# Optimization experiments

Hardware: AMD Instinct MI355X
Metric: run time of the kernel (lower is better)

Reference implementation:

```python
import jax, jax.numpy as jnp
import numpy as np

B, S, D, H = 64, 197, 1024, 4096

# I-BERT IntGELU constants: erf(x) ~ a*(x+b)^2 + c on [0,-b], integer-only form
K_SQRT2 = 1.4142          # sqrt(2)
GELU_SHIFT = 14           # 2**14 right-shift to avoid accumulator overflow
COEF_A = -0.2888
COEF_B = -1.769
COEF_C = 1.0 / COEF_A     # c folded by a, as in I-BERT (coeff[2] /= coeff[0])


def setup_inputs() -> dict:
    key = jax.random.key(0)
    k1, k2, k3, k4, k5, k6 = jax.random.split(key, 6)
    x_int = jax.random.randint(k1, (B, S, D), 0, 127).astype(jnp.int32)  # int8-range activations
    s_x = jax.random.uniform(k2, (1,), jnp.float32, 0.01, 0.03)          # per-tensor act scale
    w1 = jax.random.normal(k3, (H, D), jnp.float32) * 0.02
    b1 = jax.random.normal(k4, (H,), jnp.float32) * 0.02
    w2 = jax.random.normal(k5, (D, H), jnp.float32) * 0.02
    b2 = jax.random.normal(k6, (D,), jnp.float32) * 0.02
    return {"x_int": x_int, "s_x": s_x, "w1": w1, "b1": b1, "w2": w2, "b2": b2}


def _quant_weight(w):
    # per-tensor symmetric int8 weight quantization (QuantLinearWithWeight)
    s_w = jnp.max(jnp.abs(w)) / 127.0
    w_int = jnp.clip(jnp.round(w / s_w), -127.0, 127.0)
    return w_int, s_w


def _quant_linear(x_int, s_x, w, b):
    # integer GEMM: int8 acts x int8 weights -> int32 accumulator, scale s_x*s_w
    w_int, s_w = _quant_weight(w)
    s_out = s_x * s_w
    b_int = jnp.round(b / s_out)  # bias quantized into the accumulator scale
    acc = jnp.einsum('bsd,hd->bsh', x_int, w_int) + b_int
    return acc, s_out


def _int_erf(x_int, sf):
    # integer polynomial approx of erf (I-BERT)
    b_int = jnp.floor(COEF_B / sf)
    c_int = jnp.floor(COEF_C / sf ** 2)
    sign = jnp.sign(x_int)
    abs_int = jnp.minimum(jnp.abs(x_int), -b_int)
    y_int = sign * ((abs_int + b_int) ** 2 + c_int)
    sf_out = sf ** 2 * COEF_A
    y_int = jnp.floor(y_int / 2.0 ** GELU_SHIFT)  # shift to keep accumulator in range
    return y_int, sf_out * 2.0 ** GELU_SHIFT


def _int_gelu(x_int, sf):
    # GELU(x) = x * 0.5 * (1 + erf(x/sqrt(2))), integer-only
    sig_int, sig_sf = _int_erf(x_int, sf / K_SQRT2)
    shift_int = jnp.floor(1.0 / sig_sf)  # torch: 1.0 // sigmoid_scaling_factor
    y_int = x_int * (sig_int + shift_int)
    return y_int, sf * sig_sf / 2.0


def _quant_act(x_int, sf):
    # QuantAct: requantize int32-scale activations back to int8 (dynamic per-tensor scale)
    x_hat = x_int * sf
    s_a = jnp.max(jnp.abs(x_hat)) / 127.0
    q = jnp.clip(jnp.round(x_hat / s_a), -128.0, 127.0)
    return q, s_a


def reference(x_int, s_x, w1, b1, w2, b2):
    x = x_int.astype(jnp.float32)
    s = s_x[0]
    x, s = _quant_linear(x, s, w1, b1)   # [B,S,H] int32 accumulator
    x, s = _int_gelu(x, s)               # integer-only GELU
    x, s = _quant_act(x, s)              # requant -> int8 range
    # dropout_1 is identity in eval mode
    x, s = _quant_linear(x, s, w2, b2)   # [B,S,D] int32 accumulator
    # dropout_2 is identity in eval mode
    return x, s
```

## Files before the change

### kernel.cpp

```cpp
#include <hip/hip_runtime.h>
#include <cstdint>
#include <cstddef>

constexpr int Bb = 64, Ss = 197, Dd = 1024, Hh = 4096;
constexpr int M  = Bb * Ss;
constexpr int MT = (M + 255) / 256;
constexpr int Mpad = MT * 256;
constexpr int NBLK1 = (Hh / 256) * MT;

#define SL_S1    4
#define SL_BERF  5
#define SL_CERF  6
#define SL_SHIFT 7
#define SL_S2    8
#define SL_SA    9
#define SL_SOUT2 10
#define SL_SW1   11
#define SL_SW2   12

typedef int v4i __attribute__((ext_vector_type(4)));

#define GLD_LDS(g, l) \
  __builtin_amdgcn_global_load_lds((const __attribute__((address_space(1))) void*)(g), \
                                   (__attribute__((address_space(3))) void*)(l), 16, 0, 0)

#define PBAR() asm volatile("s_barrier" ::: "memory")
#define SCHED_FENCE() __builtin_amdgcn_sched_barrier(0)

__device__ __forceinline__ float blockmax256(float m) {
  #pragma unroll
  for (int off = 32; off; off >>= 1) m = fmaxf(m, __shfl_down(m, off, 64));
  __shared__ float wm[4];
  int lane = threadIdx.x & 63, wid = threadIdx.x >> 6;
  if (lane == 0) wm[wid] = m;
  __syncthreads();
  return fmaxf(fmaxf(wm[0], wm[1]), fmaxf(wm[2], wm[3]));
}

__global__ void k_wmax(const float* __restrict__ w1, const float* __restrict__ w2,
                       int n4, float* __restrict__ pmax) {
  int b = blockIdx.x;
  const float4* s4 = (const float4*)(b < 512 ? w1 : w2);
  float m = 0.f;
  for (int i = (b & 511) * 256 + threadIdx.x; i < n4; i += 512 * 256) {
    float4 v = s4[i];
    m = fmaxf(m, fmaxf(fmaxf(fabsf(v.x), fabsf(v.y)), fmaxf(fabsf(v.z), fabsf(v.w))));
  }
  m = blockmax256(m);
  if (threadIdx.x == 0) pmax[b] = m;
}

__global__ void k_scalars1(unsigned* slu, const float* __restrict__ pmax,
                           const float* __restrict__ s_x_ptr) {
  int t = threadIdx.x;
  float m1 = fmaxf(pmax[t], pmax[t + 256]);
  float m2 = fmaxf(pmax[512 + t], pmax[768 + t]);
  __shared__ float r1[256], r2[256];
  r1[t] = m1; r2[t] = m2;
  __syncthreads();
  for (int s = 128; s; s >>= 1) {
    if (t < s) { r1[t] = fmaxf(r1[t], r1[t + s]); r2[t] = fmaxf(r2[t], r2[t + s]); }
    __syncthreads();
  }
  if (t == 0) {
    float* slf = (float*)slu;
    float s_w1 = r1[0] / 127.0f;
    float s_w2 = r2[0] / 127.0f;
    float s1  = s_x_ptr[0] * s_w1;
    float sfe = s1 / 1.4142f;
    float berf = floorf(-1.769f / sfe);
    float cerf = floorf(((float)(1.0 / -0.2888)) / (sfe * sfe));
    float sig  = ((sfe * sfe) * -0.2888f) * 16384.0f;
    float shiftv = floorf(1.0f / sig);
    float s2 = (s1 * sig) / 2.0f;
    slf[SL_S1] = s1; slf[SL_BERF] = berf; slf[SL_CERF] = cerf;
    slf[SL_SHIFT] = shiftv; slf[SL_S2] = s2; slf[SL_SW1] = s_w1; slf[SL_SW2] = s_w2;
  }
}

__global__ void k_scalars2(unsigned* slu, const float* __restrict__ pmax,
                           float* dout_scalar) {
  int t = threadIdx.x;
  float m = 0.f;
  for (int i = t; i < NBLK1; i += 256) m = fmaxf(m, pmax[i]);
  __shared__ float r1[256];
  r1[t] = m;
  __syncthreads();
  for (int s = 128; s; s >>= 1) {
    if (t < s) r1[t] = fmaxf(r1[t], r1[t + s]);
    __syncthreads();
  }
  if (t == 0) {
    float* slf = (float*)slu;
    float xm = fabsf(r1[0] * slf[SL_S2]);
    float sa = xm / 127.0f;
    float sout2 = sa * slf[SL_SW2];
    slf[SL_SA] = sa; slf[SL_SOUT2] = sout2;
    *dout_scalar = sout2;
  }
}

__global__ void k_quantcvt(const float* __restrict__ w1, const float* __restrict__ w2,
                           const int* __restrict__ x, const unsigned* __restrict__ slu,
                           int8_t* __restrict__ w1q, int8_t* __restrict__ w2q,
                           int8_t* __restrict__ xq) {
  const float* slf = (const float*)slu;
  float sw1 = slf[SL_SW1], sw2 = slf[SL_SW2];
  const int n1 = Hh * Dd / 4, n2 = Dd * Hh / 4;
  const int nx = M * Dd / 4, n3 = Mpad * Dd / 4;
  const int total = n1 + n2 + n3;
  for (int i = blockIdx.x * blockDim.x + threadIdx.x; i < total; i += gridDim.x * blockDim.x) {
    if (i < n1 + n2) {
      bool first = i < n1;
      int idx = first ? i : i - n1;
      float sw = first ? sw1 : sw2;
      float4 v = ((const float4*)(first ? w1 : w2))[idx];
      int qa = (int)fminf(fmaxf(rintf(v.x / sw), -127.f), 127.f);
      int qb = (int)fminf(fmaxf(rintf(v.y / sw), -127.f), 127.f);
      int qc = (int)fminf(fmaxf(rintf(v.z / sw), -127.f), 127.f);
      int qd = (int)fminf(fmaxf(rintf(v.w / sw), -127.f), 127.f);
      unsigned p = (unsigned)(qa & 0xff) | ((unsigned)(qb & 0xff) << 8) |
                   ((unsigned)(qc & 0xff) << 16) | ((unsigned)(qd & 0xff) << 24);
      ((unsigned*)(first ? w1q : w2q))[idx] = p;
    } else {
      int idx = i - n1 - n2;
      unsigned p = 0u;
      if (idx < nx) {
        int4 v = ((const int4*)x)[idx];
        p = (unsigned)(v.x & 0xff) | ((unsigned)(v.y & 0xff) << 8) |
            ((unsigned)(v.z & 0xff) << 16) | ((unsigned)(v.w & 0xff) << 24);
      }
      ((unsigned*)xq)[idx] = p;
    }
  }
}

template <int K, int MODE>
__global__ __launch_bounds__(512, 2) void k_gemm(
    const int8_t* __restrict__ A, const int8_t* __restrict__ Bm,
    const float* __restrict__ bias, const unsigned* __restrict__ slu,
    int8_t* __restrict__ qout, float* __restrict__ fout, float* __restrict__ pmax_y,
    int Mreal, int Ncols) {
  constexpr int NK = K / 128;
  __shared__ alignas(64) int8_t smem[131072];
  const int t = threadIdx.x;
  const int bm = blockIdx.y, bn = blockIdx.x;
  const int lane = t & 63, wid = t >> 6;
  const int wr = wid >> 2, wc = wid & 3;
  const int lm = lane & 15, quad = lane >> 4;

  const int srow = t >> 2;
  const int scc  = (t & 3) ^ ((srow >> 1) & 3);
  const int8_t* aSrc = A  + (size_t)(bm * 256 + srow) * K + scc * 16;
  const int8_t* bSrc = Bm + (size_t)(bn * 256 + srow) * K + scc * 16;

  int aoff[8], boff[4];
  #pragma unroll
  for (int i = 0; i < 8; i++) {
    int r = wr * 128 + i * 16 + lm;
    aoff[i] = r * 64 + ((quad ^ ((r >> 1) & 3)) << 4);
  }
  #pragma unroll
  for (int j = 0; j < 4; j++) {
    int r = wc * 64 + j * 16 + lm;
    boff[j] = r * 64 + ((quad ^ ((r >> 1) & 3)) << 4);
  }

  v4i acc[8][4] = {};

  auto stA = [&](int buf, int kt, int ks) {
    int8_t* d = smem + buf * 65536 + ks * 16384 + t * 16;
    const int8_t* s = aSrc + kt * 128 + ks * 64;
    GLD_LDS(s, d);
    GLD_LDS(s + (size_t)128 * K, d + 8192);
  };
  auto stB = [&](int buf, int kt, int ks) {
    int8_t* d = smem + buf * 65536 + 32768 + ks * 16384 + t * 16;
    const int8_t* s = bSrc + kt * 128 + ks * 64;
    GLD_LDS(s, d);
    GLD_LDS(s + (size_t)128 * K, d + 8192);
  };

  stB(0, 0, 0); stA(0, 0, 0); stB(0, 0, 1); stA(0, 0, 1);
  asm volatile("s_waitcnt vmcnt(4)" ::: "memory");
  SCHED_FENCE();
  PBAR();

  #pragma unroll 1
  for (int kt = 0; kt < NK; ++kt) {
    const int cb = kt & 1, nb = cb ^ 1;
    const int8_t* Ac = smem + cb * 65536;
    const int8_t* Bc = Ac + 32768;
    const bool pf = (kt + 1 < NK);
    v4i bf[4], af[4];

    #pragma unroll
    for (int j = 0; j < 4; j++) bf[j] = *(const v4i*)(Bc + boff[j]);
    #pragma unroll
    for (int i = 0; i < 4; i++) af[i] = *(const v4i*)(Ac + aoff[i]);
    if (pf) stB(nb, kt + 1, 0);
    PBAR();
    __builtin_amdgcn_s_setprio(1);
    #pragma unroll
    for (int i = 0; i < 4; i++)
      #pragma unroll
      for (int j = 0; j < 4; j++)
        acc[i][j] = __builtin_amdgcn_mfma_i32_16x16x64_i8(bf[j], af[i], acc[i][j], 0, 0, 0);
    __builtin_amdgcn_s_setprio(0);
    SCHED_FENCE();
    PBAR();

    #pragma unroll
    for (int i = 0; i < 4; i++) af[i] = *(const v4i*)(Ac + aoff[4 + i]);
    if (pf) stA(nb, kt + 1, 0);
    PBAR();
    __builtin_amdgcn_s_setprio(1);
    #pragma unroll
    for (int i = 0; i < 4; i++)
      #pragma unroll
      for (int j = 0; j < 4; j++)
        acc[4 + i][j] = __builtin_amdgcn_mfma_i32_16x16x64_i8(bf[j], af[i], acc[4 + i][j], 0, 0, 0);
    __builtin_amdgcn_s_setprio(0);
    if (pf) asm volatile("s_waitcnt vmcnt(4)" ::: "memory");
    else    asm volatile("s_waitcnt vmcnt(0)" ::: "memory");
    SCHED_FENCE();
    PBAR();

    #pragma unroll
    for (int j = 0; j < 4; j++) bf[j] = *(const v4i*)(Bc + 16384 + boff[j]);
    #pragma unroll
    for (int i = 0; i < 4; i++) af[i] = *(const v4i*)(Ac + 16384 + aoff[i]);
    if (pf) stB(nb, kt + 1, 1);
    PBAR();
    __builtin_amdgcn_s_setprio(1);
    #pragma unroll
    for (int i = 0; i < 4; i++)
      #pragma unroll
      for (int j = 0; j < 4; j++)
        acc[i][j] = __builtin_amdgcn_mfma_i32_16x16x64_i8(bf[j], af[i], acc[i][j], 0, 0, 0);
    __builtin_amdgcn_s_setprio(0);
    SCHED_FENCE();
    PBAR();

    #pragma unroll
    for (int i = 0; i < 4; i++) af[i] = *(const v4i*)(Ac + 16384 + aoff[4 + i]);
    if (pf) stA(nb, kt + 1, 1);
    PBAR();
    __builtin_amdgcn_s_setprio(1);
    #pragma unroll
    for (int i = 0; i < 4; i++)
      #pragma unroll
      for (int j = 0; j < 4; j++)
        acc[4 + i][j] = __builtin_amdgcn_mfma_i32_16x16x64_i8(bf[j], af[i], acc[4 + i][j], 0, 0, 0);
    __builtin_amdgcn_s_setprio(0);
    if (pf) asm volatile("s_waitcnt vmcnt(4)" ::: "memory");
    else    asm volatile("s_waitcnt vmcnt(0)" ::: "memory");
    SCHED_FENCE();
    PBAR();
  }

  const float* slf = (const float*)slu;
  if constexpr (MODE == 2) {
    float sout2 = slf[SL_SOUT2];
    float4 bq[4];
    #pragma unroll
    for (int j = 0; j < 4; j++) {
      float4 bv = *(const float4*)(bias + bn * 256 + wc * 64 + j * 16 + quad * 4);
      bq[j].x = rintf(bv.x / sout2); bq[j].y = rintf(bv.y / sout2);
      bq[j].z = rintf(bv.z / sout2); bq[j].w = rintf(bv.w / sout2);
    }
    #pragma unroll
    for (int i = 0; i < 8; i++) {
      int gr = bm * 256 + wr * 128 + i * 16 + lm;
      if (gr < Mreal) {
        #pragma unroll
        for (int j = 0; j < 4; j++) {
          int gc0 = bn * 256 + wc * 64 + j * 16 + quad * 4;
          float4 o;
          o.x = (float)acc[i][j][0] + bq[j].x;
          o.y = (float)acc[i][j][1] + bq[j].y;
          o.z = (float)acc[i][j][2] + bq[j].z;
          o.w = (float)acc[i][j][3] + bq[j].w;
          *(float4*)(fout + (size_t)gr * Ncols + gc0) = o;
        }
      }
    }
  } else {
    float s1 = slf[SL_S1], berf = slf[SL_BERF], cerf = slf[SL_CERF], shiftv = slf[SL_SHIFT];
    float s2 = slf[SL_S2];
    float sa = (MODE == 1) ? slf[SL_SA] : 1.0f;
    float r_req = (MODE == 1) ? (s2 / sa) : 1.0f;
    float lmax = 0.f;
    float4 bq[4];
    #pragma unroll
    for (int j = 0; j < 4; j++) {
      float4 bv = *(const float4*)(bias + bn * 256 + wc * 64 + j * 16 + quad * 4);
      bq[j].x = rintf(bv.x / s1); bq[j].y = rintf(bv.y / s1);
      bq[j].z = rintf(bv.z / s1); bq[j].w = rintf(bv.w / s1);
    }
    #pragma unroll
    for (int i = 0; i < 8; i++) {
      int mrow = wr * 128 + i * 16 + lm;
      int gr = bm * 256 + mrow;
      bool rowok = gr < Mreal;
      #pragma unroll
      for (int j = 0; j < 4; j++) {
        int n0 = wc * 64 + j * 16 + quad * 4;
        unsigned packed = 0u;
        #pragma unroll
        for (int r = 0; r < 4; r++) {
          float a = (float)acc[i][j][r] + ((const float*)&bq[j])[r];
          float ax = fminf(fabsf(a), -berf);
          float tt = ax + berf;
          float u = tt * tt + cerf;
          float ye = (a < 0.f) ? -u : u;
          float yv = floorf(ye * (1.0f / 16384.0f));
          float y = a * (yv + shiftv);
          if constexpr (MODE == 0) {
            if (rowok) lmax = fmaxf(lmax, fabsf(y));
          } else {
            float qf = rintf(y * r_req);
            qf = fminf(fmaxf(qf, -128.f), 127.f);
            packed |= ((unsigned)((int)qf & 0xff)) << (8 * r);
          }
        }
        if constexpr (MODE == 1) {
          *(unsigned*)(smem + mrow * 272 + n0) = packed;
        }
      }
    }
    if constexpr (MODE == 0) {
      #pragma unroll
      for (int off = 32; off; off >>= 1) lmax = fmaxf(lmax, __shfl_down(lmax, off, 64));
      float* red = (float*)smem;
      if (lane == 0) red[wid] = lmax;
      __syncthreads();
      if (t == 0) {
        float b = fmaxf(fmaxf(fmaxf(red[0], red[1]), fmaxf(red[2], red[3])),
                        fmaxf(fmaxf(red[4], red[5]), fmaxf(red[6], red[7])));
        pmax_y[bm * gridDim.x + bn] = b;
      }
    } else {
      __syncthreads();
      #pragma unroll
      for (int c2 = 0; c2 < 8; c2++) {
        int idx = c2 * 512 + t;
        int row = idx >> 4, c16 = (idx & 15) << 4;
        v4i v = *(const v4i*)(smem + row * 272 + c16);
        *(v4i*)(qout + (size_t)(bm * 256 + row) * Ncols + bn * 256 + c16) = v;
      }
    }
  }
}

extern "C" void kernel_launch(void* const* d_in, const int* in_sizes, int n_in,
                              void* d_out, int out_size, void* d_ws, size_t ws_size,
                              hipStream_t stream) {
  const int*   x   = (const int*)d_in[0];
  const float* s_x = (const float*)d_in[1];
  const float* w1  = (const float*)d_in[2];
  const float* b1  = (const float*)d_in[3];
  const float* w2  = (const float*)d_in[4];
  const float* b2  = (const float*)d_in[5];
  float* out = (float*)d_out;

  char* ws = (char*)d_ws;
  unsigned* slots = (unsigned*)ws;
  float* pmax_w = (float*)(ws + 1024);
  float* pmax_y = (float*)(ws + 8192);
  int8_t* w1q = (int8_t*)(ws + 32768);
  int8_t* w2q = w1q + (size_t)Hh * Dd;
  int8_t* xq  = w2q + (size_t)Dd * Hh;
  int8_t* qbuf = xq + (size_t)Mpad * Dd;

  k_wmax<<<1024, 256, 0, stream>>>(w1, w2, Hh * Dd / 4, pmax_w);
  k_scalars1<<<1, 256, 0, stream>>>(slots, pmax_w, s_x);
  k_quantcvt<<<1024, 256, 0, stream>>>(w1, w2, x, slots, w1q, w2q, xq);

  dim3 g1(Hh / 256, MT);
  k_gemm<Dd, 0><<<g1, 512, 0, stream>>>(xq, w1q, b1, slots, nullptr, nullptr,
                                        pmax_y, M, Hh);
  k_scalars2<<<1, 256, 0, stream>>>(slots, pmax_y, out + (size_t)M * Dd);
  k_gemm<Dd, 1><<<g1, 512, 0, stream>>>(xq, w1q, b1, slots, qbuf, nullptr,
                                        nullptr, M, Hh);
  dim3 g2(Dd / 256, MT);
  k_gemm<Hh, 2><<<g2, 512, 0, stream>>>(qbuf, w2q, b2, slots, nullptr, out,
                                        nullptr, M, Dd);
}
```

Baseline: 383.9 us.

## Replace double-buffered interleaved GEMM pipeline with single-buffer 256-wide K tiles

Replaces the fine-grained double-buffered K loop (128-wide K tiles in two 64-wide halves, each load interleaved with MFMA work under raw barriers) with a single buffer holding 256-wide K tiles. The whole tile is loaded with 16-byte swizzled async copies, the kernel waits and syncs, runs all MFMAs, syncs again, and only then issues the next load. This makes the loop simpler and halves the number of iterations, but global loads no longer overlap with compute, so memory latency is exposed on every tile.

```diff
diff --git a/kernel.cpp b/kernel.cpp
--- a/kernel.cpp
+++ b/kernel.cpp
@@ -23,9 +23,6 @@
 #define GLD_LDS(g, l) \
   __builtin_amdgcn_global_load_lds((const __attribute__((address_space(1))) void*)(g), \
                                    (__attribute__((address_space(3))) void*)(l), 16, 0, 0)
-
-#define PBAR() asm volatile("s_barrier" ::: "memory")
-#define SCHED_FENCE() __builtin_amdgcn_sched_barrier(0)
 
 __device__ __forceinline__ float blockmax256(float m) {
   #pragma unroll
@@ -141,7 +138,7 @@
     const float* __restrict__ bias, const unsigned* __restrict__ slu,
     int8_t* __restrict__ qout, float* __restrict__ fout, float* __restrict__ pmax_y,
     int Mreal, int Ncols) {
-  constexpr int NK = K / 128;
+  constexpr int NK = K / 256;
   __shared__ alignas(64) int8_t smem[131072];
   const int t = threadIdx.x;
   const int bm = blockIdx.y, bn = blockIdx.x;
@@ -149,114 +146,65 @@
   const int wr = wid >> 2, wc = wid & 3;
   const int lm = lane & 15, quad = lane >> 4;
 
-  const int srow = t >> 2;
-  const int scc  = (t & 3) ^ ((srow >> 1) & 3);
-  const int8_t* aSrc = A  + (size_t)(bm * 256 + srow) * K + scc * 16;
-  const int8_t* bSrc = Bm + (size_t)(bn * 256 + srow) * K + scc * 16;
-
-  int aoff[8], boff[4];
+  const int srow0 = t >> 4;
+  const int gcol  = (t & 15) ^ (srow0 & 7);
+  const int8_t* aSrc = A  + (size_t)(bm * 256 + srow0) * K + gcol * 16;
+  const int8_t* bSrc = Bm + (size_t)(bn * 256 + srow0) * K + gcol * 16;
+
+  v4i acc[8][4] = {};
+
+  auto stage = [&](int kt) {
+    const size_t ko = (size_t)kt * 256;
+    #pragma unroll
+    for (int j = 0; j < 8; j++) {
+      GLD_LDS(aSrc + (size_t)(32 * j) * K + ko, smem + (j * 512 + t) * 16);
+      GLD_LDS(bSrc + (size_t)(32 * j) * K + ko, smem + 65536 + (j * 512 + t) * 16);
+    }
+  };
+
+  int arow[8], ar7[8], brow[4], br7[4];
   #pragma unroll
   for (int i = 0; i < 8; i++) {
     int r = wr * 128 + i * 16 + lm;
-    aoff[i] = r * 64 + ((quad ^ ((r >> 1) & 3)) << 4);
+    arow[i] = r * 256; ar7[i] = r & 7;
   }
   #pragma unroll
   for (int j = 0; j < 4; j++) {
     int r = wc * 64 + j * 16 + lm;
-    boff[j] = r * 64 + ((quad ^ ((r >> 1) & 3)) << 4);
-  }
-
-  v4i acc[8][4] = {};
-
-  auto stA = [&](int buf, int kt, int ks) {
-    int8_t* d = smem + buf * 65536 + ks * 16384 + t * 16;
-    const int8_t* s = aSrc + kt * 128 + ks * 64;
-    GLD_LDS(s, d);
-    GLD_LDS(s + (size_t)128 * K, d + 8192);
-  };
-  auto stB = [&](int buf, int kt, int ks) {
-    int8_t* d = smem + buf * 65536 + 32768 + ks * 16384 + t * 16;
-    const int8_t* s = bSrc + kt * 128 + ks * 64;
-    GLD_LDS(s, d);
-    GLD_LDS(s + (size_t)128 * K, d + 8192);
-  };
-
-  stB(0, 0, 0); stA(0, 0, 0); stB(0, 0, 1); stA(0, 0, 1);
-  asm volatile("s_waitcnt vmcnt(4)" ::: "memory");
-  SCHED_FENCE();
-  PBAR();
+    brow[j] = r * 256; br7[j] = r & 7;
+  }
+
+  stage(0);
 
   #pragma unroll 1
   for (int kt = 0; kt < NK; ++kt) {
-    const int cb = kt & 1, nb = cb ^ 1;
-    const int8_t* Ac = smem + cb * 65536;
-    const int8_t* Bc = Ac + 32768;
-    const bool pf = (kt + 1 < NK);
-    v4i bf[4], af[4];
-
-    #pragma unroll
-    for (int j = 0; j < 4; j++) bf[j] = *(const v4i*)(Bc + boff[j]);
-    #pragma unroll
-    for (int i = 0; i < 4; i++) af[i] = *(const v4i*)(Ac + aoff[i]);
-    if (pf) stB(nb, kt + 1, 0);
-    PBAR();
+    asm volatile("s_waitcnt vmcnt(0)");
+    __syncthreads();
+    const int8_t* As = smem;
+    const int8_t* Bs = smem + 65536;
     __builtin_amdgcn_s_setprio(1);
     #pragma unroll
-    for (int i = 0; i < 4; i++)
-      #pragma unroll
-      for (int j = 0; j < 4; j++)
-        acc[i][j] = __builtin_amdgcn_mfma_i32_16x16x64_i8(bf[j], af[i], acc[i][j], 0, 0, 0);
+    for (int ksub = 0; ksub < 4; ksub++) {
+      v4i af[8], bf[4];
+      #pragma unroll
+      for (int j = 0; j < 4; j++) {
+        int pc = ((ksub << 2) | quad) ^ br7[j];
+        bf[j] = *(const v4i*)(Bs + brow[j] + (pc << 4));
+      }
+      #pragma unroll
+      for (int i = 0; i < 8; i++) {
+        int pc = ((ksub << 2) | quad) ^ ar7[i];
+        af[i] = *(const v4i*)(As + arow[i] + (pc << 4));
+      }
+      #pragma unroll
+      for (int i = 0; i < 8; i++)
+        #pragma unroll
+        for (int j = 0; j < 4; j++)
+          acc[i][j] = __builtin_amdgcn_mfma_i32_16x16x64_i8(bf[j], af[i], acc[i][j], 0, 0, 0);
+    }
     __builtin_amdgcn_s_setprio(0);
-    SCHED_FENCE();
-    PBAR();
-
-    #pragma unroll
-    for (int i = 0; i < 4; i++) af[i] = *(const v4i*)(Ac + aoff[4 + i]);
-    if (pf) stA(nb, kt + 1, 0);
-    PBAR();
-    __builtin_amdgcn_s_setprio(1);
-    #pragma unroll
-    for (int i = 0; i < 4; i++)
-      #pragma unroll
-      for (int j = 0; j < 4; j++)
-        acc[4 + i][j] = __builtin_amdgcn_mfma_i32_16x16x64_i8(bf[j], af[i], acc[4 + i][j], 0, 0, 0);
-    __builtin_amdgcn_s_setprio(0);
-    if (pf) asm volatile("s_waitcnt vmcnt(4)" ::: "memory");
-    else    asm volatile("s_waitcnt vmcnt(0)" ::: "memory");
-    SCHED_FENCE();
-    PBAR();
-
-    #pragma unroll
-    for (int j = 0; j < 4; j++) bf[j] = *(const v4i*)(Bc + 16384 + boff[j]);
-    #pragma unroll
-    for (int i = 0; i < 4; i++) af[i] = *(const v4i*)(Ac + 16384 + aoff[i]);
-    if (pf) stB(nb, kt + 1, 1);
-    PBAR();
-    __builtin_amdgcn_s_setprio(1);
-    #pragma unroll
-    for (int i = 0; i < 4; i++)
-      #pragma unroll
-      for (int j = 0; j < 4; j++)
-        acc[i][j] = __builtin_amdgcn_mfma_i32_16x16x64_i8(bf[j], af[i], acc[i][j], 0, 0, 0);
-    __builtin_amdgcn_s_setprio(0);
-    SCHED_FENCE();
-    PBAR();
-
-    #pragma unroll
-    for (int i = 0; i < 4; i++) af[i] = *(const v4i*)(Ac + 16384 + aoff[4 + i]);
-    if (pf) stA(nb, kt + 1, 1);
-    PBAR();
-    __builtin_amdgcn_s_setprio(1);
-    #pragma unroll
-    for (int i = 0; i < 4; i++)
-      #pragma unroll
-      for (int j = 0; j < 4; j++)
-        acc[4 + i][j] = __builtin_amdgcn_mfma_i32_16x16x64_i8(bf[j], af[i], acc[4 + i][j], 0, 0, 0);
-    __builtin_amdgcn_s_setprio(0);
-    if (pf) asm volatile("s_waitcnt vmcnt(4)" ::: "memory");
-    else    asm volatile("s_waitcnt vmcnt(0)" ::: "memory");
-    SCHED_FENCE();
-    PBAR();
+    __syncthreads();
+    if (kt + 1 < NK) stage(kt + 1);
   }
 
   const float* slf = (const float*)slu;
```

After: 410.7 us. 7.0% more time.
